# Performance work log

Hardware: AMD Instinct MI355X
Metric: run time of the kernel (lower is better)

Reference implementation:

```python
import jax, jax.numpy as jnp
import numpy as np

D_MODEL = 1024
N_HEADS = 16
HEAD_DIM = D_MODEL // N_HEADS
SCALE = HEAD_DIM ** -0.5  # 0.125


def setup_inputs() -> dict:
    key = jax.random.key(0)
    k1, k2, k3, k4 = jax.random.split(key, 4)
    B, H, S, d = 2, N_HEADS, 2048, HEAD_DIM
    q = jax.random.normal(k1, (B, H, S, d), dtype=jnp.float32)
    k = jax.random.normal(k2, (B, H, d, S), dtype=jnp.float32)  # pre-transposed, as in torch.matmul(q, k)
    v = jax.random.normal(k3, (B, H, S, d), dtype=jnp.float32)
    prev = jax.random.normal(k4, (B, H, S, S), dtype=jnp.float32)
    return {"q": q, "k": k, "v": v, "prev": prev}


def reference(q, k, v, prev):
    # attn_scores = (q @ k) * scale + prev   (scores must be returned pre-softmax)
    attn_scores = jnp.einsum("bhsd,bhdt->bhst", q, k) * SCALE + prev
    attn_weights = jax.nn.softmax(attn_scores, axis=-1)
    # dropout p=0.0 -> identity (module default / eval)
    out = jnp.einsum("bhst,bhtd->bhsd", attn_weights, v)
    return (out, attn_scores)
```

## Files before the change

kernel.cpp:

```cpp
#include <hip/hip_runtime.h>
#include <hip/hip_fp16.h>


typedef _Float16 half8 __attribute__((ext_vector_type(8)));
typedef _Float16 half4v __attribute__((ext_vector_type(4)));
typedef float f32x4 __attribute__((ext_vector_type(4)));

constexpr int S_LEN = 2048;
constexpr int DHEAD = 64;
constexpr int BH_TOT = 32;
constexpr float SCALE = 0.125f;
constexpr float LOG2E = 1.4426950408889634f;
constexpr float M_FIX = 8.0f * LOG2E;

__global__ __launch_bounds__(256) void tconv(const float* __restrict__ in,
                                             _Float16* __restrict__ outp,
                                             int R, int C) {
    const int head = blockIdx.z;
    const int r0 = blockIdx.y * 64, c0 = blockIdx.x * 64;
    const float* src = in + (size_t)head * R * C;
    _Float16* dst = outp + (size_t)head * R * C;
    __shared__ _Float16 t[64][68];
    const int tx = threadIdx.x & 63;
    const int ty = threadIdx.x >> 6;
    #pragma unroll
    for (int i = 0; i < 16; ++i) {
        const int rr = ty + i * 4;
        t[tx][rr] = (_Float16)src[(size_t)(r0 + rr) * C + c0 + tx];
    }
    __syncthreads();
    const int cw = threadIdx.x >> 4;
    const int dx = (threadIdx.x & 15) * 4;
    #pragma unroll
    for (int i = 0; i < 4; ++i) {
        const int crow = cw + i * 16;
        half4v vv;
        #pragma unroll
        for (int j = 0; j < 4; ++j) vv[j] = t[crow][dx + j];
        *reinterpret_cast<half4v*>(&dst[(size_t)(c0 + crow) * R + r0 + dx]) = vv;
    }
}

__global__ __launch_bounds__(256, 4) void attn_fused(
    const float* __restrict__ q, const float* __restrict__ prev,
    const _Float16* __restrict__ k16t, const _Float16* __restrict__ v16t,
    float* __restrict__ out, float* __restrict__ scores)
{
    const int tid = threadIdx.x;
    const int lane = tid & 63;
    const int wave = tid >> 6;
    const int lg = lane >> 4;
    const int lr = lane & 15;

    const int bid = blockIdx.x;
    const int swz = (bid & 7) * 128 + (bid >> 3);
    const int bh = swz >> 5;
    const int rb = swz & 31;
    const int i0 = rb * 64 + wave * 16;

    const float* qh = q + (size_t)bh * S_LEN * DHEAD;
    const float* ph = prev + (size_t)bh * S_LEN * S_LEN;
    float* sh = scores + (size_t)bh * S_LEN * S_LEN;
    float* oh = out + (size_t)bh * S_LEN * DHEAD;
    const _Float16* kt = k16t + (size_t)bh * S_LEN * DHEAD;
    const _Float16* vt = v16t + (size_t)bh * S_LEN * DHEAD;

    __shared__ __align__(16) _Float16 sbuf[2][4096];
    __shared__ __align__(16) _Float16 p_lds[4][16][40];

    const int sr = tid >> 3;
    const int s8 = tid & 7;
    const size_t srcKoff = (size_t)sr * DHEAD + (size_t)((s8 ^ (sr & 7)) * 8);
    const int vd = tid >> 2;
    const int v4 = tid & 3;
    const size_t srcVoff = (size_t)vd * S_LEN + (size_t)(((v4 ^ ((vd >> 1) & 3)) * 8));
    _Float16* const dKA = &sbuf[0][tid * 8];
    _Float16* const dKB = &sbuf[1][tid * 8];
    _Float16* const dVA = &sbuf[0][2048 + tid * 8];
    _Float16* const dVB = &sbuf[1][2048 + tid * 8];

    half8 qa[2];
    {
        const float* qrow = qh + (size_t)(i0 + lr) * DHEAD + lg * 8;
        #pragma unroll
        for (int h = 0; h < 2; ++h) {
            half8 t;
            #pragma unroll
            for (int e = 0; e < 8; ++e) t[e] = (_Float16)qrow[h * 32 + e];
            qa[h] = t;
        }
    }

    f32x4 acc[4] = {};
    float lsum[4] = {0.f, 0.f, 0.f, 0.f};

    auto load_prev = [&](int jt, float (&P)[8]) {
        #pragma unroll
        for (int r = 0; r < 4; ++r) {
            const size_t rowoff = (size_t)(i0 + lg * 4 + r) * S_LEN + jt + lr;
            P[r * 2]     = ph[rowoff];
            P[r * 2 + 1] = ph[rowoff + 16];
        }
    };

    half8 RK, RV;

    auto step = [&](int t, float (&P)[8]) {
        const int b = t & 1;
        *reinterpret_cast<half8*>(b ? dKA : dKB) = RK;
        *reinterpret_cast<half8*>(b ? dVA : dVB) = RV;
        const int tn = (t + 2 < 64) ? t + 2 : 63;
        RK = *reinterpret_cast<const half8*>(kt + (size_t)(tn * 32) * DHEAD + srcKoff);
        RV = *reinterpret_cast<const half8*>(vt + (size_t)(tn * 32) + srcVoff);

        const _Float16* kB = &sbuf[b][0];
        half8 kb[4];
        #pragma unroll
        for (int s = 0; s < 2; ++s) {
            const int r = s * 16 + lr;
            #pragma unroll
            for (int h = 0; h < 2; ++h)
                kb[s * 2 + h] = *reinterpret_cast<const half8*>(
                    kB + r * 64 + (((h * 4 + lg) ^ (lr & 7)) * 8));
        }
        f32x4 sacc[2] = {};
        __builtin_amdgcn_s_setprio(1);
        sacc[0] = __builtin_amdgcn_mfma_f32_16x16x32_f16(qa[0], kb[0], sacc[0], 0, 0, 0);
        sacc[0] = __builtin_amdgcn_mfma_f32_16x16x32_f16(qa[1], kb[1], sacc[0], 0, 0, 0);
        sacc[1] = __builtin_amdgcn_mfma_f32_16x16x32_f16(qa[0], kb[2], sacc[1], 0, 0, 0);
        sacc[1] = __builtin_amdgcn_mfma_f32_16x16x32_f16(qa[1], kb[3], sacc[1], 0, 0, 0);
        __builtin_amdgcn_s_setprio(0);

        const int jt = t * 32;
        #pragma unroll
        for (int r = 0; r < 4; ++r) {
            const int row = lg * 4 + r;
            const size_t rowoff = (size_t)(i0 + row) * S_LEN + jt + lr;
            const float a0 = fmaf(sacc[0][r], SCALE, P[r * 2]);
            const float a1 = fmaf(sacc[1][r], SCALE, P[r * 2 + 1]);
            sh[rowoff] = a0;
            sh[rowoff + 16] = a1;
            const float p0 = exp2f(fmaf(a0, LOG2E, -M_FIX));
            const float p1 = exp2f(fmaf(a1, LOG2E, -M_FIX));
            lsum[r] += p0 + p1;
            p_lds[wave][row][lr]      = (_Float16)p0;
            p_lds[wave][row][lr + 16] = (_Float16)p1;
        }
        load_prev(tn * 32, P);

        const half8 pa = *reinterpret_cast<const half8*>(&p_lds[wave][lr][lg * 8]);
        __builtin_amdgcn_s_setprio(1);
        #pragma unroll
        for (int f = 0; f < 4; ++f) {
            const int d = f * 16 + lr;
            const half8 vb = *reinterpret_cast<const half8*>(
                kB + 2048 + d * 32 + ((lg ^ ((lr >> 1) & 3)) * 8));
            acc[f] = __builtin_amdgcn_mfma_f32_16x16x32_f16(pa, vb, acc[f], 0, 0, 0);
        }
        __builtin_amdgcn_s_setprio(0);

        asm volatile("s_waitcnt lgkmcnt(0)" ::: "memory");
        __builtin_amdgcn_s_barrier();
        asm volatile("" ::: "memory");
    };

    float PA[8], PB[8];
    RK = *reinterpret_cast<const half8*>(kt + srcKoff);
    RV = *reinterpret_cast<const half8*>(vt + srcVoff);
    *reinterpret_cast<half8*>(dKA) = RK;
    *reinterpret_cast<half8*>(dVA) = RV;
    RK = *reinterpret_cast<const half8*>(kt + (size_t)32 * DHEAD + srcKoff);
    RV = *reinterpret_cast<const half8*>(vt + (size_t)32 + srcVoff);
    load_prev(0, PA);
    load_prev(32, PB);
    asm volatile("s_waitcnt lgkmcnt(0)" ::: "memory");
    __builtin_amdgcn_s_barrier();
    asm volatile("" ::: "memory");

    for (int t = 0; t < 64; t += 2) {
        step(t, PA);
        step(t + 1, PB);
    }

    #pragma unroll
    for (int r = 0; r < 4; ++r) {
        float s = lsum[r];
        s += __shfl_xor(s, 1);
        s += __shfl_xor(s, 2);
        s += __shfl_xor(s, 4);
        s += __shfl_xor(s, 8);
        const float inv = 1.0f / s;
        const size_t o = (size_t)(i0 + lg * 4 + r) * DHEAD + lr;
        #pragma unroll
        for (int f = 0; f < 4; ++f)
            oh[o + f * 16] = acc[f][r] * inv;
    }
}

__global__ __launch_bounds__(256, 4) void attn_fallback(
    const float* __restrict__ q, const float* __restrict__ k,
    const float* __restrict__ v, const float* __restrict__ prev,
    float* __restrict__ out, float* __restrict__ scores)
{
    const int lane = threadIdx.x & 63;
    const int wave = threadIdx.x >> 6;
    const int lg = lane >> 4, lr = lane & 15;
    const int bh = blockIdx.x >> 5;
    const int rowblk = blockIdx.x & 31;
    const int i0 = rowblk * 64 + wave * 16;

    const float* qh = q + (size_t)bh * S_LEN * DHEAD;
    const float* kh = k + (size_t)bh * DHEAD * S_LEN;
    const float* vh = v + (size_t)bh * S_LEN * DHEAD;
    const float* ph = prev + (size_t)bh * S_LEN * S_LEN;
    float* sh = scores + (size_t)bh * S_LEN * S_LEN;
    float* oh = out + (size_t)bh * S_LEN * DHEAD;

    __shared__ __align__(16) _Float16 p_lds[4][16][40];

    half8 qa[2];
    {
        const float* qrow = qh + (size_t)(i0 + lr) * DHEAD + lg * 8;
        #pragma unroll
        for (int h = 0; h < 2; ++h) {
            half8 t;
            #pragma unroll
            for (int e = 0; e < 8; ++e) t[e] = (_Float16)qrow[h * 32 + e];
            qa[h] = t;
        }
    }
    f32x4 acc[4] = {};
    float lsum[4] = {0.f, 0.f, 0.f, 0.f};

    for (int jt = 0; jt < S_LEN; jt += 32) {
        half8 kb[4], vb[4];
        #pragma unroll
        for (int h = 0; h < 2; ++h)
            #pragma unroll
            for (int s = 0; s < 2; ++s) {
                const float* kp = kh + (size_t)(h * 32 + lg * 8) * S_LEN + jt + s * 16 + lr;
                half8 t;
                #pragma unroll
                for (int e = 0; e < 8; ++e) t[e] = (_Float16)kp[(size_t)e * S_LEN];
                kb[s * 2 + h] = t;
            }
        #pragma unroll
        for (int f = 0; f < 4; ++f) {
            const float* vp = vh + (size_t)(jt + lg * 8) * DHEAD + f * 16 + lr;
            half8 t;
            #pragma unroll
            for (int e = 0; e < 8; ++e) t[e] = (_Float16)vp[(size_t)e * DHEAD];
            vb[f] = t;
        }
        f32x4 sacc[2] = {};
        sacc[0] = __builtin_amdgcn_mfma_f32_16x16x32_f16(qa[0], kb[0], sacc[0], 0, 0, 0);
        sacc[0] = __builtin_amdgcn_mfma_f32_16x16x32_f16(qa[1], kb[1], sacc[0], 0, 0, 0);
        sacc[1] = __builtin_amdgcn_mfma_f32_16x16x32_f16(qa[0], kb[2], sacc[1], 0, 0, 0);
        sacc[1] = __builtin_amdgcn_mfma_f32_16x16x32_f16(qa[1], kb[3], sacc[1], 0, 0, 0);
        #pragma unroll
        for (int r = 0; r < 4; ++r) {
            const size_t rowoff = (size_t)(i0 + lg * 4 + r) * S_LEN + jt + lr;
            const float a0 = fmaf(sacc[0][r], SCALE, ph[rowoff]);
            const float a1 = fmaf(sacc[1][r], SCALE, ph[rowoff + 16]);
            sh[rowoff] = a0;
            sh[rowoff + 16] = a1;
            const float p0 = exp2f(fmaf(a0, LOG2E, -M_FIX));
            const float p1 = exp2f(fmaf(a1, LOG2E, -M_FIX));
            lsum[r] += p0 + p1;
            p_lds[wave][lg * 4 + r][lr]      = (_Float16)p0;
            p_lds[wave][lg * 4 + r][lr + 16] = (_Float16)p1;
        }
        const half8 pa = *reinterpret_cast<const half8*>(&p_lds[wave][lr][lg * 8]);
        #pragma unroll
        for (int f = 0; f < 4; ++f)
            acc[f] = __builtin_amdgcn_mfma_f32_16x16x32_f16(pa, vb[f], acc[f], 0, 0, 0);
    }
    #pragma unroll
    for (int r = 0; r < 4; ++r) {
        float s = lsum[r];
        s += __shfl_xor(s, 1);
        s += __shfl_xor(s, 2);
        s += __shfl_xor(s, 4);
        s += __shfl_xor(s, 8);
        const float inv = 1.0f / s;
        const size_t o = (size_t)(i0 + lg * 4 + r) * DHEAD + lr;
        #pragma unroll
        for (int f = 0; f < 4; ++f)
            oh[o + f * 16] = acc[f][r] * inv;
    }
}

extern "C" void kernel_launch(void* const* d_in, const int* in_sizes, int n_in,
                              void* d_out, int out_size, void* d_ws, size_t ws_size,
                              hipStream_t stream) {
    const float* q    = (const float*)d_in[0];
    const float* k    = (const float*)d_in[1];
    const float* v    = (const float*)d_in[2];
    const float* prev = (const float*)d_in[3];
    float* out = (float*)d_out;
    float* scores = out + (size_t)BH_TOT * S_LEN * DHEAD;

    const size_t elems = (size_t)BH_TOT * S_LEN * DHEAD;
    const size_t need = 2 * elems * sizeof(_Float16);

    if (d_ws != nullptr && ws_size >= need) {
        _Float16* k16t = (_Float16*)d_ws;
        _Float16* v16t = k16t + elems;
        tconv<<<dim3(S_LEN / 64, DHEAD / 64, BH_TOT), 256, 0, stream>>>(k, k16t, DHEAD, S_LEN);
        tconv<<<dim3(DHEAD / 64, S_LEN / 64, BH_TOT), 256, 0, stream>>>(v, v16t, S_LEN, DHEAD);
        attn_fused<<<dim3(1024), dim3(256), 0, stream>>>(q, prev, k16t, v16t, out, scores);
    } else {
        attn_fallback<<<dim3(1024), dim3(256), 0, stream>>>(q, k, v, prev, out, scores);
    }
}
```

Baseline: 283.4 us.

## Shrink attention blocks to two waves and double the grid

```diff
diff --git a/kernel.cpp b/kernel.cpp
--- a/kernel.cpp
+++ b/kernel.cpp
@@ -41,7 +41,7 @@
     }
 }
 
-__global__ __launch_bounds__(256, 4) void attn_fused(
+__global__ __launch_bounds__(128, 4) void attn_fused(
     const float* __restrict__ q, const float* __restrict__ prev,
     const _Float16* __restrict__ k16t, const _Float16* __restrict__ v16t,
     float* __restrict__ out, float* __restrict__ scores)
@@ -53,10 +53,10 @@
     const int lr = lane & 15;
 
     const int bid = blockIdx.x;
-    const int swz = (bid & 7) * 128 + (bid >> 3);
-    const int bh = swz >> 5;
-    const int rb = swz & 31;
-    const int i0 = rb * 64 + wave * 16;
+    const int swz = (bid & 7) * 256 + (bid >> 3);
+    const int bh = swz >> 6;
+    const int rb = swz & 63;
+    const int i0 = rb * 32 + wave * 16;
 
     const float* qh = q + (size_t)bh * S_LEN * DHEAD;
     const float* ph = prev + (size_t)bh * S_LEN * S_LEN;
@@ -66,18 +66,13 @@
     const _Float16* vt = v16t + (size_t)bh * S_LEN * DHEAD;
 
     __shared__ __align__(16) _Float16 sbuf[2][4096];
-    __shared__ __align__(16) _Float16 p_lds[4][16][40];
-
-    const int sr = tid >> 3;
-    const int s8 = tid & 7;
-    const size_t srcKoff = (size_t)sr * DHEAD + (size_t)((s8 ^ (sr & 7)) * 8);
-    const int vd = tid >> 2;
-    const int v4 = tid & 3;
-    const size_t srcVoff = (size_t)vd * S_LEN + (size_t)(((v4 ^ ((vd >> 1) & 3)) * 8));
-    _Float16* const dKA = &sbuf[0][tid * 8];
-    _Float16* const dKB = &sbuf[1][tid * 8];
-    _Float16* const dVA = &sbuf[0][2048 + tid * 8];
-    _Float16* const dVB = &sbuf[1][2048 + tid * 8];
+    __shared__ __align__(16) _Float16 p_lds[2][16][40];
+
+    const int c0 = tid, c1 = tid + 128;
+    const size_t srcK0 = (size_t)(c0 >> 3) * DHEAD + (size_t)((((c0 & 7) ^ ((c0 >> 3) & 7)) * 8));
+    const size_t srcK1 = (size_t)(c1 >> 3) * DHEAD + (size_t)((((c1 & 7) ^ ((c1 >> 3) & 7)) * 8));
+    const size_t srcV0 = (size_t)(c0 >> 2) * S_LEN + (size_t)((((c0 & 3) ^ ((c0 >> 3) & 3)) * 8));
+    const size_t srcV1 = (size_t)(c1 >> 2) * S_LEN + (size_t)((((c1 & 3) ^ ((c1 >> 3) & 3)) * 8));
 
     half8 qa[2];
     {
@@ -103,15 +98,29 @@
         }
     };
 
-    half8 RK, RV;
+    half8 RK0, RK1, RV0, RV1;
+
+    auto refill = [&](int tn) {
+        const _Float16* kbase = kt + (size_t)(tn * 32) * DHEAD;
+        const _Float16* vbase = vt + (size_t)(tn * 32);
+        RK0 = *reinterpret_cast<const half8*>(kbase + srcK0);
+        RK1 = *reinterpret_cast<const half8*>(kbase + srcK1);
+        RV0 = *reinterpret_cast<const half8*>(vbase + srcV0);
+        RV1 = *reinterpret_cast<const half8*>(vbase + srcV1);
+    };
+    auto publish = [&](int buf) {
+        _Float16* base = &sbuf[buf][0];
+        *reinterpret_cast<half8*>(base + c0 * 8) = RK0;
+        *reinterpret_cast<half8*>(base + c1 * 8) = RK1;
+        *reinterpret_cast<half8*>(base + 2048 + c0 * 8) = RV0;
+        *reinterpret_cast<half8*>(base + 2048 + c1 * 8) = RV1;
+    };
 
     auto step = [&](int t, float (&P)[8]) {
         const int b = t & 1;
-        *reinterpret_cast<half8*>(b ? dKA : dKB) = RK;
-        *reinterpret_cast<half8*>(b ? dVA : dVB) = RV;
+        publish(b ^ 1);
         const int tn = (t + 2 < 64) ? t + 2 : 63;
-        RK = *reinterpret_cast<const half8*>(kt + (size_t)(tn * 32) * DHEAD + srcKoff);
-        RV = *reinterpret_cast<const half8*>(vt + (size_t)(tn * 32) + srcVoff);
+        refill(tn);
 
         const _Float16* kB = &sbuf[b][0];
         half8 kb[4];
@@ -165,12 +174,9 @@
     };
 
     float PA[8], PB[8];
-    RK = *reinterpret_cast<const half8*>(kt + srcKoff);
-    RV = *reinterpret_cast<const half8*>(vt + srcVoff);
-    *reinterpret_cast<half8*>(dKA) = RK;
-    *reinterpret_cast<half8*>(dVA) = RV;
-    RK = *reinterpret_cast<const half8*>(kt + (size_t)32 * DHEAD + srcKoff);
-    RV = *reinterpret_cast<const half8*>(vt + (size_t)32 + srcVoff);
+    refill(0);
+    publish(0);
+    refill(1);
     load_prev(0, PA);
     load_prev(32, PB);
     asm volatile("s_waitcnt lgkmcnt(0)" ::: "memory");
@@ -308,7 +314,7 @@
         _Float16* v16t = k16t + elems;
         tconv<<<dim3(S_LEN / 64, DHEAD / 64, BH_TOT), 256, 0, stream>>>(k, k16t, DHEAD, S_LEN);
         tconv<<<dim3(DHEAD / 64, S_LEN / 64, BH_TOT), 256, 0, stream>>>(v, v16t, S_LEN, DHEAD);
-        attn_fused<<<dim3(1024), dim3(256), 0, stream>>>(q, prev, k16t, v16t, out, scores);
+        attn_fused<<<dim3(2048), dim3(128), 0, stream>>>(q, prev, k16t, v16t, out, scores);
     } else {
         attn_fallback<<<dim3(1024), dim3(256), 0, stream>>>(q, k, v, prev, out, scores);
     }
```

Result: slower. 344.5 us (+21.6%).

## Stage K/V tiles with direct global-to-LDS loads instead of register staging

Applied to the files above, without the earlier changes.

```diff
diff --git a/kernel.cpp b/kernel.cpp
--- a/kernel.cpp
+++ b/kernel.cpp
@@ -41,6 +41,12 @@
     }
 }
 
+__device__ __forceinline__ void gl2lds16h(const _Float16* g, _Float16* l) {
+    __builtin_amdgcn_global_load_lds(
+        (const __attribute__((address_space(1))) void*)g,
+        (__attribute__((address_space(3))) void*)l, 16, 0, 0);
+}
+
 __global__ __launch_bounds__(256, 4) void attn_fused(
     const float* __restrict__ q, const float* __restrict__ prev,
     const _Float16* __restrict__ k16t, const _Float16* __restrict__ v16t,
@@ -68,16 +74,16 @@
     __shared__ __align__(16) _Float16 sbuf[2][4096];
     __shared__ __align__(16) _Float16 p_lds[4][16][40];
 
-    const int sr = tid >> 3;
-    const int s8 = tid & 7;
-    const size_t srcKoff = (size_t)sr * DHEAD + (size_t)((s8 ^ (sr & 7)) * 8);
-    const int vd = tid >> 2;
-    const int v4 = tid & 3;
-    const size_t srcVoff = (size_t)vd * S_LEN + (size_t)(((v4 ^ ((vd >> 1) & 3)) * 8));
-    _Float16* const dKA = &sbuf[0][tid * 8];
-    _Float16* const dKB = &sbuf[1][tid * 8];
-    _Float16* const dVA = &sbuf[0][2048 + tid * 8];
-    _Float16* const dVB = &sbuf[1][2048 + tid * 8];
+    const int ck = wave * 64 + lane;
+    const size_t srcKoff = (size_t)(ck >> 3) * DHEAD
+                         + (size_t)((((ck & 7) ^ ((ck >> 3) & 7)) * 8));
+    const size_t srcVoff = (size_t)(ck >> 2) * S_LEN
+                         + (size_t)((((ck & 3) ^ ((ck >> 3) & 3)) * 8));
+
+    auto stage = [&](int tn, int buf) {
+        gl2lds16h(kt + (size_t)(tn * 32) * DHEAD + srcKoff, &sbuf[buf][wave * 512]);
+        gl2lds16h(vt + (size_t)(tn * 32) + srcVoff, &sbuf[buf][2048 + wave * 512]);
+    };
 
     half8 qa[2];
     {
@@ -103,15 +109,10 @@
         }
     };
 
-    half8 RK, RV;
-
     auto step = [&](int t, float (&P)[8]) {
         const int b = t & 1;
-        *reinterpret_cast<half8*>(b ? dKA : dKB) = RK;
-        *reinterpret_cast<half8*>(b ? dVA : dVB) = RV;
-        const int tn = (t + 2 < 64) ? t + 2 : 63;
-        RK = *reinterpret_cast<const half8*>(kt + (size_t)(tn * 32) * DHEAD + srcKoff);
-        RV = *reinterpret_cast<const half8*>(vt + (size_t)(tn * 32) + srcVoff);
+        stage((t + 1 < 64) ? t + 1 : 63, b ^ 1);
+        __builtin_amdgcn_sched_barrier(0);
 
         const _Float16* kB = &sbuf[b][0];
         half8 kb[4];
@@ -146,6 +147,7 @@
             p_lds[wave][row][lr]      = (_Float16)p0;
             p_lds[wave][row][lr + 16] = (_Float16)p1;
         }
+        const int tn = (t + 2 < 64) ? t + 2 : 63;
         load_prev(tn * 32, P);
 
         const half8 pa = *reinterpret_cast<const half8*>(&p_lds[wave][lr][lg * 8]);
@@ -159,21 +161,16 @@
         }
         __builtin_amdgcn_s_setprio(0);
 
-        asm volatile("s_waitcnt lgkmcnt(0)" ::: "memory");
+        asm volatile("s_waitcnt vmcnt(16)" ::: "memory");
         __builtin_amdgcn_s_barrier();
         asm volatile("" ::: "memory");
     };
 
     float PA[8], PB[8];
-    RK = *reinterpret_cast<const half8*>(kt + srcKoff);
-    RV = *reinterpret_cast<const half8*>(vt + srcVoff);
-    *reinterpret_cast<half8*>(dKA) = RK;
-    *reinterpret_cast<half8*>(dVA) = RV;
-    RK = *reinterpret_cast<const half8*>(kt + (size_t)32 * DHEAD + srcKoff);
-    RV = *reinterpret_cast<const half8*>(vt + (size_t)32 + srcVoff);
+    stage(0, 0);
     load_prev(0, PA);
     load_prev(32, PB);
-    asm volatile("s_waitcnt lgkmcnt(0)" ::: "memory");
+    asm volatile("s_waitcnt vmcnt(0)" ::: "memory");
     __builtin_amdgcn_s_barrier();
     asm volatile("" ::: "memory");
 
```

Result: no change. 281.7 us (-0.6%).
